# Optimization experiments

Measured on AMD Instinct MI355X. Metric: run time of the kernel, lower is better.

## Reference

```python
import jax, jax.numpy as jnp
import numpy as np

B, S, D = 4, 2048, 1024
H, DK = 16, 64
NUM_BUCKETS = 32
MAX_DISTANCE = 128
EPS = 1e-6


def _relative_position_bucket(q_len, kv_len):
    # causal (bidirectional=False) T5 bucketization
    ctx = jnp.arange(q_len, dtype=jnp.int32)[:, None]
    mem = jnp.arange(kv_len, dtype=jnp.int32)[None, :]
    rp = mem - ctx                       # [q, kv]
    rp = -jnp.minimum(rp, 0)             # nonnegative distances to the past
    max_exact = NUM_BUCKETS // 2
    is_small = rp < max_exact
    rp_safe = jnp.maximum(rp, 1).astype(jnp.float32)
    large = max_exact + (
        jnp.log(rp_safe / max_exact) / np.log(MAX_DISTANCE / max_exact) * (NUM_BUCKETS - max_exact)
    ).astype(jnp.int32)
    large = jnp.minimum(large, NUM_BUCKETS - 1)
    return jnp.where(is_small, rp, large)  # [q, kv] int32 in [0, NUM_BUCKETS)


def setup_inputs() -> dict:
    key = jax.random.key(0)
    k1, k2, k3, k4 = jax.random.split(key, 4)
    hidden_states = jax.random.normal(k1, (B, S, D), dtype=jnp.float32)
    sequence_mask = jnp.ones((B, S), dtype=bool)
    rms_w = jnp.ones((D,), dtype=jnp.float32)
    W_qkv = jax.random.normal(k2, (D, 3 * H * DK), dtype=jnp.float32) * (D ** -0.5)
    W_o = jax.random.normal(k3, (H * DK, D), dtype=jnp.float32) * ((H * DK) ** -0.5)
    rel_bias = jax.random.normal(k4, (NUM_BUCKETS, H), dtype=jnp.float32)
    return {"hidden_states": hidden_states, "sequence_mask": sequence_mask,
            "rms_w": rms_w, "W_qkv": W_qkv, "W_o": W_o, "rel_bias": rel_bias}


def reference(hidden_states, sequence_mask, rms_w, W_qkv, W_o, rel_bias):
    # RMSNorm
    var = jnp.mean(hidden_states * hidden_states, axis=-1, keepdims=True)
    normed = hidden_states * jax.lax.rsqrt(var + EPS) * rms_w

    # QKV projection -> [B, S, 3, H, DK] -> [B, H, S, DK] each
    qkv = (normed @ W_qkv).reshape(B, S, 3, H, DK)
    q = jnp.transpose(qkv[:, :, 0], (0, 2, 1, 3))
    k = jnp.transpose(qkv[:, :, 1], (0, 2, 1, 3))
    v = jnp.transpose(qkv[:, :, 2], (0, 2, 1, 3))

    # relative position bias: gather [S,S,H] -> [1,H,S,S]
    bucket = _relative_position_bucket(S, S)
    pos_bias = jnp.transpose(rel_bias[bucket], (2, 0, 1))[None]

    # scores (note: T5 does NOT scale by 1/sqrt(dk))
    scores = jnp.einsum("bhqd,bhkd->bhqk", q, k) + pos_bias

    # causal mask combined with sequence mask (True = attend)
    causal = jnp.tril(jnp.ones((S, S), dtype=bool))
    mask = causal[None, None] & sequence_mask[:, None, None, :]
    scores = jnp.where(mask, scores, jnp.finfo(scores.dtype).min)

    attn = jax.nn.softmax(scores.astype(jnp.float32), axis=-1).astype(scores.dtype)
    # dropout p=0 / eval mode -> identity
    ctx = jnp.einsum("bhqk,bhkd->bhqd", attn, v)          # [B,H,S,DK]
    ctx = jnp.transpose(ctx, (0, 2, 1, 3)).reshape(B, S, H * DK)
    out = hidden_states + ctx @ W_o                        # residual
    return out
```

## Files before the change

### kernel.cpp

```cpp
#include <hip/hip_runtime.h>
#include <math.h>


typedef unsigned short ushort_t;
typedef __attribute__((ext_vector_type(8))) short bfrag;
typedef __attribute__((ext_vector_type(4))) float ffrag;

#define MFMA16(a, b, c) __builtin_amdgcn_mfma_f32_16x16x32_bf16((a), (b), (c), 0, 0, 0)
#define LOG2E 1.4426950408889634f

__device__ __forceinline__ void load_lds16(const ushort_t* g, ushort_t* l) {
  __builtin_amdgcn_global_load_lds(
      (const __attribute__((address_space(1))) unsigned int*)g,
      (__attribute__((address_space(3))) unsigned int*)l, 16, 0, 0);
}

__device__ __forceinline__ ushort_t f2bf(float f) {
  union { float f; unsigned u; } x; x.f = f;
  unsigned r = x.u + 0x7FFFu + ((x.u >> 16) & 1u);
  return (ushort_t)(r >> 16);
}
__device__ __forceinline__ float bf2f(ushort_t u) {
  union { unsigned u; float f; } x; x.u = ((unsigned)u) << 16; return x.f;
}
__device__ __forceinline__ unsigned cvtpk(float lo, float hi) {
  unsigned r;
  asm("v_cvt_pk_bf16_f32 %0, %1, %2" : "=v"(r) : "v"(lo), "v"(hi));
  return r;
}
__device__ __forceinline__ float exp2fast(float x) {
  return __builtin_amdgcn_exp2f(x);
}

__global__ __launch_bounds__(256) void norm_cvt_kernel(
    const float* __restrict__ hidden, const float* __restrict__ rms_w,
    ushort_t* __restrict__ normed) {
  const int w = threadIdx.x >> 6, lane = threadIdx.x & 63;
  const int row = blockIdx.x * 4 + w;
  const float* p = hidden + (size_t)row * 1024;
  float4 v[4];
  float s = 0.f;
#pragma unroll
  for (int i = 0; i < 4; ++i) {
    v[i] = *(const float4*)(p + (lane + i * 64) * 4);
    s += v[i].x * v[i].x + v[i].y * v[i].y + v[i].z * v[i].z + v[i].w * v[i].w;
  }
#pragma unroll
  for (int off = 1; off < 64; off <<= 1) s += __shfl_xor(s, off, 64);
  const float scale = rsqrtf(s * (1.0f / 1024.0f) + 1e-6f);
#pragma unroll
  for (int i = 0; i < 4; ++i) {
    const int c0 = (lane + i * 64) * 4;
    float4 wv = *(const float4*)(rms_w + c0);
    ushort4 u;
    u.x = f2bf(v[i].x * scale * wv.x);
    u.y = f2bf(v[i].y * scale * wv.y);
    u.z = f2bf(v[i].z * scale * wv.z);
    u.w = f2bf(v[i].w * scale * wv.w);
    *(ushort4*)(normed + (size_t)row * 1024 + c0) = u;
  }
}

__global__ __launch_bounds__(256) void transpose_cvt_kernel(
    const float* __restrict__ in, ushort_t* __restrict__ out, int R, int C) {
  __shared__ float tile[32][33];
  const int r0 = blockIdx.y * 32, c0 = blockIdx.x * 32;
  const int tr = threadIdx.x >> 5, tc = threadIdx.x & 31;
#pragma unroll
  for (int i = 0; i < 32; i += 8)
    tile[tr + i][tc] = in[(size_t)(r0 + tr + i) * C + c0 + tc];
  __syncthreads();
#pragma unroll
  for (int i = 0; i < 32; i += 8)
    out[(size_t)(c0 + tr + i) * R + r0 + tc] = f2bf(tile[tc][tr + i]);
}

__global__ __launch_bounds__(256, 2) void qkv_mfma_kernel(
    const ushort_t* __restrict__ A, const ushort_t* __restrict__ Bt,
    ushort_t* __restrict__ qbf, ushort_t* __restrict__ kbf,
    ushort_t* __restrict__ vtbf) {
  __shared__ ushort_t As[2][128][64];
  __shared__ ushort_t Bs[2][128][64];
  const int tid = threadIdx.x, lane = tid & 63, w = tid >> 6;
  const int quad = lane >> 4, ln = lane & 15;
  const int wr = w >> 1, wc = w & 1;
  const int id = blockIdx.x;
  const int xcd = id & 7, t8 = id >> 3;
  const int by = xcd * 8 + t8 / 24, bx = t8 % 24;
  const int m0 = by * 128, n0 = bx * 128;
  const int rswz = ln & 7;

  auto stage = [&](const ushort_t* src, ushort_t* lds, int gr0, int gc0) {
#pragma unroll
    for (int i = 0; i < 4; ++i) {
      const int idx = i * 256 + tid;
      const int r = idx >> 3, c = idx & 7;
      load_lds16(src + (size_t)(gr0 + r) * 1024 + gc0 + ((c ^ (r & 7)) * 8),
                 lds + idx * 8);
    }
  };

  ffrag acc[4][4];
#pragma unroll
  for (int i = 0; i < 4; ++i)
#pragma unroll
    for (int j = 0; j < 4; ++j) acc[i][j] = (ffrag)0.f;

  stage(A, &As[0][0][0], m0, 0);
  stage(Bt, &Bs[0][0][0], n0, 0);
  asm volatile("s_waitcnt vmcnt(0)" ::: "memory");
  __builtin_amdgcn_s_barrier();

  for (int t = 0; t < 16; ++t) {
    const int cur = t & 1;
    if (t + 1 < 16) {
      stage(A, &As[cur ^ 1][0][0], m0, (t + 1) * 64);
      stage(Bt, &Bs[cur ^ 1][0][0], n0, (t + 1) * 64);
    }
    bfrag a[4][2], b[4][2];
#pragma unroll
    for (int mi = 0; mi < 4; ++mi) {
      const int rA = wr * 64 + mi * 16 + ln;
#pragma unroll
      for (int ks = 0; ks < 2; ++ks)
        a[mi][ks] = *(const bfrag*)(&As[cur][rA][((ks * 4 + quad) ^ rswz) * 8]);
    }
#pragma unroll
    for (int ni = 0; ni < 4; ++ni) {
      const int rB = wc * 64 + ni * 16 + ln;
#pragma unroll
      for (int ks = 0; ks < 2; ++ks)
        b[ni][ks] = *(const bfrag*)(&Bs[cur][rB][((ks * 4 + quad) ^ rswz) * 8]);
    }
    __builtin_amdgcn_s_setprio(1);
#pragma unroll
    for (int mi = 0; mi < 4; ++mi)
#pragma unroll
      for (int ni = 0; ni < 4; ++ni)
#pragma unroll
        for (int ks = 0; ks < 2; ++ks)
          acc[mi][ni] = MFMA16(a[mi][ks], b[ni][ks], acc[mi][ni]);
    __builtin_amdgcn_s_setprio(0);
    asm volatile("s_waitcnt vmcnt(0)" ::: "memory");
    __builtin_amdgcn_s_barrier();
  }

  const int b_idx = m0 >> 11;
  const int cbase = n0 + wc * 64 + ln;
#pragma unroll
  for (int mi = 0; mi < 4; ++mi) {
    const int sbase = (m0 & 2047) + wr * 64 + mi * 16 + quad * 4;
#pragma unroll
    for (int ni = 0; ni < 4; ++ni) {
      const int c = cbase + ni * 16;
      const int three = c >> 10, rem = c & 1023;
      const int h = rem >> 6, dk = rem & 63;
      if (three == 2) {
        ushort4 u;
        u.x = f2bf(acc[mi][ni][0]); u.y = f2bf(acc[mi][ni][1]);
        u.z = f2bf(acc[mi][ni][2]); u.w = f2bf(acc[mi][ni][3]);
        *(ushort4*)(vtbf + ((size_t)(b_idx * 16 + h) * 64 + dk) * 2048 + sbase) = u;
      } else {
        const float sc = (three == 0) ? 1.0f : LOG2E;
        ushort_t* dst = (three == 0 ? qbf : kbf) +
                        ((size_t)(b_idx * 16 + h) * 2048 + sbase) * 64 + dk;
        dst[0]   = f2bf(acc[mi][ni][0] * sc);
        dst[64]  = f2bf(acc[mi][ni][1] * sc);
        dst[128] = f2bf(acc[mi][ni][2] * sc);
        dst[192] = f2bf(acc[mi][ni][3] * sc);
      }
    }
  }
}

__global__ __launch_bounds__(256, 3) void attn_mfma_kernel(
    const ushort_t* __restrict__ qbf, const ushort_t* __restrict__ kbf,
    const ushort_t* __restrict__ vtbf, const float* __restrict__ rel_bias,
    ushort_t* __restrict__ ctx) {
  __shared__ ushort_t Kt[2][2][64][32];
  __shared__ ushort_t Vt[2][2][64][32];
  __shared__ ushort_t Pt[128][64];
  __shared__ ushort_t bias_t[2048];

  const int tid = threadIdx.x, w = tid >> 6, lane = tid & 63;
  const int quad = lane >> 4, ln = lane & 15;
  const int id = blockIdx.x;
  const int bh = id & 63;
  const int qb = 15 - (id >> 6);
  const int h = bh & 15;
  const int nt = 2 * qb + 2;
  const int q0w = qb * 128 + w * 32;

  for (int dist = tid; dist < 2048; dist += 256) {
    int bucket;
    if (dist < 16) bucket = dist;
    else {
      bucket = 16 + (int)(logf((float)dist * (1.0f / 16.0f)) * (16.0f / logf(8.0f)));
      if (bucket > 31) bucket = 31;
    }
    bias_t[dist] = f2bf(rel_bias[bucket * 16 + h] * LOG2E);
  }
  const float c31 = bf2f(f2bf(rel_bias[31 * 16 + h] * LOG2E));
  __syncthreads();

  const size_t khead = (size_t)bh * 2048 * 64;
  const int rsw = ((ln >> 1) & 3) * 8;
  const int psw = (ln & 7) * 8;

  bfrag aq[2][2];
#pragma unroll
  for (int ni = 0; ni < 2; ++ni)
#pragma unroll
    for (int kf = 0; kf < 2; ++kf)
      aq[ni][kf] = *(const bfrag*)(qbf + ((size_t)bh * 2048 + q0w + ni * 16 + ln) * 64 +
                                   kf * 32 + quad * 8);

  bfrag ones;
#pragma unroll
  for (int i = 0; i < 8; ++i) ones[i] = (short)0x3F80;

  ffrag o[2][4], l_acc[2];
#pragma unroll
  for (int mo = 0; mo < 2; ++mo) {
#pragma unroll
    for (int nd = 0; nd < 4; ++nd) o[mo][nd] = (ffrag)0.f;
    l_acc[mo] = (ffrag)0.f;
  }
  float m_run[2] = {-3.0e38f, -3.0e38f};

  auto stageKV = [&](int key0, int buf) {
#pragma unroll
    for (int i = 0; i < 2; ++i) {
      const int cid = i * 256 + tid;
      const int kf = cid >> 8, row = (cid >> 2) & 63, c8 = cid & 3;
      const int sw = (c8 ^ ((row >> 1) & 3)) * 8;
      load_lds16(kbf + khead + (size_t)(key0 + row) * 64 + kf * 32 + sw,
                 &Kt[buf][0][0][0] + cid * 8);
      load_lds16(vtbf + khead + (size_t)row * 2048 + key0 + kf * 32 + sw,
                 &Vt[buf][0][0][0] + cid * 8);
    }
  };

  stageKV(0, 0);

  int cur = 0;
  for (int j = 0; j < nt; ++j) {
    const int key0 = j * 64;
    asm volatile("s_waitcnt vmcnt(0)" ::: "memory");
    __builtin_amdgcn_s_barrier();

    if (j + 1 < nt) stageKV(key0 + 64, cur ^ 1);

    if (key0 <= q0w + 31) {
      ffrag s[4][2];
#pragma unroll
      for (int mi = 0; mi < 4; ++mi)
#pragma unroll
        for (int ni = 0; ni < 2; ++ni) s[mi][ni] = (ffrag)0.f;
      __builtin_amdgcn_s_setprio(1);
#pragma unroll
      for (int kf = 0; kf < 2; ++kf)
#pragma unroll
        for (int mi = 0; mi < 4; ++mi) {
          bfrag ak = *(const bfrag*)&Kt[cur][kf][mi * 16 + ln][(quad * 8) ^ rsw];
          s[mi][0] = MFMA16(ak, aq[0][kf], s[mi][0]);
          s[mi][1] = MFMA16(ak, aq[1][kf], s[mi][1]);
        }
      __builtin_amdgcn_s_setprio(0);

      const bool fastT = (key0 + 176 <= q0w);
      float sbias = 0.f;
      if (fastT) {
        sbias = c31;
      } else {
#pragma unroll
        for (int ni = 0; ni < 2; ++ni) {
          const int q = q0w + ni * 16 + ln;
          if (key0 + 63 > q0w + ni * 16) {
#pragma unroll
            for (int mi = 0; mi < 4; ++mi) {
              const int keyb = key0 + mi * 16 + quad * 4;
#pragma unroll
              for (int r = 0; r < 4; ++r) {
                const int dist = q - (keyb + r);
                const int db = dist < 0 ? 0 : dist;
                s[mi][ni][r] = (dist < 0) ? -3.0e38f
                                          : (s[mi][ni][r] + bf2f(bias_t[db]));
              }
            }
          } else {
#pragma unroll
            for (int mi = 0; mi < 4; ++mi) {
              const int keyb = key0 + mi * 16 + quad * 4;
#pragma unroll
              for (int r = 0; r < 4; ++r)
                s[mi][ni][r] += bf2f(bias_t[q - (keyb + r)]);
            }
          }
        }
      }

      float mxl[2];
#pragma unroll
      for (int ni = 0; ni < 2; ++ni) {
        float a0 = fmaxf(fmaxf(s[0][ni][0], s[0][ni][1]), fmaxf(s[0][ni][2], s[0][ni][3]));
        float a1 = fmaxf(fmaxf(s[1][ni][0], s[1][ni][1]), fmaxf(s[1][ni][2], s[1][ni][3]));
        float a2 = fmaxf(fmaxf(s[2][ni][0], s[2][ni][1]), fmaxf(s[2][ni][2], s[2][ni][3]));
        float a3 = fmaxf(fmaxf(s[3][ni][0], s[3][ni][1]), fmaxf(s[3][ni][2], s[3][ni][3]));
        mxl[ni] = fmaxf(fmaxf(a0, a1), fmaxf(a2, a3)) + sbias;
      }

      if (!__all(mxl[0] <= m_run[0] + 8.0f && mxl[1] <= m_run[1] + 8.0f)) {
#pragma unroll
        for (int ni = 0; ni < 2; ++ni) {
          float mx = mxl[ni];
          mx = fmaxf(mx, __shfl_xor(mx, 16, 64));
          mx = fmaxf(mx, __shfl_xor(mx, 32, 64));
          const float mnew = fmaxf(m_run[ni], mx);
          const float alpha = exp2fast(m_run[ni] - mnew);
          m_run[ni] = mnew;
#pragma unroll
          for (int r = 0; r < 4; ++r) {
            const float af = __shfl(alpha, quad * 4 + r, 64);
#pragma unroll
            for (int nd = 0; nd < 4; ++nd) o[ni][nd][r] *= af;
            l_acc[ni][r] *= af;
          }
        }
      }
#pragma unroll
      for (int ni = 0; ni < 2; ++ni) {
        const float sh = m_run[ni] - sbias;
#pragma unroll
        for (int mi = 0; mi < 4; ++mi)
#pragma unroll
          for (int r = 0; r < 4; ++r)
            s[mi][ni][r] = exp2fast(s[mi][ni][r] - sh);
      }

#pragma unroll
      for (int ni = 0; ni < 2; ++ni) {
        ushort_t* prow = &Pt[w * 32 + ni * 16 + ln][0];
#pragma unroll
        for (int mi = 0; mi < 4; ++mi) {
          uint2 pk;
          pk.x = cvtpk(s[mi][ni][0], s[mi][ni][1]);
          pk.y = cvtpk(s[mi][ni][2], s[mi][ni][3]);
          *(uint2*)(prow + ((mi * 16 + quad * 4) ^ psw)) = pk;
        }
      }

      __builtin_amdgcn_s_setprio(1);
#pragma unroll
      for (int kf = 0; kf < 2; ++kf) {
        bfrag ap0 = *(const bfrag*)&Pt[w * 32 + ln][(kf * 32 + quad * 8) ^ psw];
        bfrag ap1 = *(const bfrag*)&Pt[w * 32 + 16 + ln][(kf * 32 + quad * 8) ^ psw];
        l_acc[0] = MFMA16(ap0, ones, l_acc[0]);
        l_acc[1] = MFMA16(ap1, ones, l_acc[1]);
#pragma unroll
        for (int nd = 0; nd < 4; ++nd) {
          bfrag bv = *(const bfrag*)&Vt[cur][kf][nd * 16 + ln][(quad * 8) ^ rsw];
          o[0][nd] = MFMA16(ap0, bv, o[0][nd]);
          o[1][nd] = MFMA16(ap1, bv, o[1][nd]);
        }
      }
      __builtin_amdgcn_s_setprio(0);
    }
    cur ^= 1;
  }

#pragma unroll
  for (int mo = 0; mo < 2; ++mo) {
    ffrag inv;
#pragma unroll
    for (int r = 0; r < 4; ++r) inv[r] = 1.0f / l_acc[mo][r];
    const int s0 = q0w + mo * 16 + quad * 4;
#pragma unroll
    for (int nd = 0; nd < 4; ++nd)
#pragma unroll
      for (int r = 0; r < 4; ++r)
        ctx[((size_t)(bh >> 4) * 2048 + s0 + r) * 1024 + h * 64 + nd * 16 + ln] =
            f2bf(o[mo][nd][r] * inv[r]);
  }
}

__global__ __launch_bounds__(256, 2) void out_mfma_kernel(
    const ushort_t* __restrict__ A, const ushort_t* __restrict__ Bt,
    const float* __restrict__ hidden, float* __restrict__ out) {
  __shared__ ushort_t As[2][128][64];
  __shared__ ushort_t Bs[2][128][64];
  const int tid = threadIdx.x, lane = tid & 63, w = tid >> 6;
  const int quad = lane >> 4, ln = lane & 15;
  const int wr = w >> 1, wc = w & 1;
  const int id = blockIdx.x;
  const int xcd = id & 7, t = id >> 3;
  const int by = xcd * 8 + (t >> 3), bx = t & 7;
  const int m0 = by * 128, n0 = bx * 128;
  const int rswz = ln & 7;

  auto stage = [&](const ushort_t* src, ushort_t* lds, int gr0, int gc0) {
#pragma unroll
    for (int i = 0; i < 4; ++i) {
      const int idx = i * 256 + tid;
      const int r = idx >> 3, c = idx & 7;
      load_lds16(src + (size_t)(gr0 + r) * 1024 + gc0 + ((c ^ (r & 7)) * 8),
                 lds + idx * 8);
    }
  };

  ffrag acc[4][4];
#pragma unroll
  for (int i = 0; i < 4; ++i)
#pragma unroll
    for (int j = 0; j < 4; ++j) acc[i][j] = (ffrag)0.f;

  stage(A, &As[0][0][0], m0, 0);
  stage(Bt, &Bs[0][0][0], n0, 0);
  asm volatile("s_waitcnt vmcnt(0)" ::: "memory");
  __builtin_amdgcn_s_barrier();

  for (int t2 = 0; t2 < 16; ++t2) {
    const int cur = t2 & 1;
    if (t2 + 1 < 16) {
      stage(A, &As[cur ^ 1][0][0], m0, (t2 + 1) * 64);
      stage(Bt, &Bs[cur ^ 1][0][0], n0, (t2 + 1) * 64);
    }
    bfrag a[4][2], b[4][2];
#pragma unroll
    for (int mi = 0; mi < 4; ++mi) {
      const int rA = wr * 64 + mi * 16 + ln;
#pragma unroll
      for (int ks = 0; ks < 2; ++ks)
        a[mi][ks] = *(const bfrag*)(&As[cur][rA][((ks * 4 + quad) ^ rswz) * 8]);
    }
#pragma unroll
    for (int ni = 0; ni < 4; ++ni) {
      const int rB = wc * 64 + ni * 16 + ln;
#pragma unroll
      for (int ks = 0; ks < 2; ++ks)
        b[ni][ks] = *(const bfrag*)(&Bs[cur][rB][((ks * 4 + quad) ^ rswz) * 8]);
    }
    __builtin_amdgcn_s_setprio(1);
#pragma unroll
    for (int mi = 0; mi < 4; ++mi)
#pragma unroll
      for (int ni = 0; ni < 4; ++ni)
#pragma unroll
        for (int ks = 0; ks < 2; ++ks)
          acc[mi][ni] = MFMA16(a[mi][ks], b[ni][ks], acc[mi][ni]);
    __builtin_amdgcn_s_setprio(0);
    asm volatile("s_waitcnt vmcnt(0)" ::: "memory");
    __builtin_amdgcn_s_barrier();
  }

#pragma unroll
  for (int mi = 0; mi < 4; ++mi) {
    const int m = m0 + wr * 64 + mi * 16 + quad * 4;
#pragma unroll
    for (int ni = 0; ni < 4; ++ni) {
      const int c = n0 + wc * 64 + ni * 16 + ln;
#pragma unroll
      for (int r = 0; r < 4; ++r) {
        const size_t off = (size_t)(m + r) * 1024 + c;
        out[off] = acc[mi][ni][r] + hidden[off];
      }
    }
  }
}

extern "C" void kernel_launch(void* const* d_in, const int* in_sizes, int n_in,
                              void* d_out, int out_size, void* d_ws, size_t ws_size,
                              hipStream_t stream) {
  const size_t NORMED = (size_t)8192 * 1024;
  const size_t WQKVT  = (size_t)3072 * 1024;
  const size_t WOT    = (size_t)1024 * 1024;
  const size_t QKVE   = (size_t)64 * 2048 * 64;
  const size_t need = (NORMED + WQKVT + WOT + 3 * QKVE + NORMED) * 2;
  if (ws_size < need) return;

  const float* hidden   = (const float*)d_in[0];
  const float* rms_w    = (const float*)d_in[2];
  const float* Wqkv     = (const float*)d_in[3];
  const float* Wo       = (const float*)d_in[4];
  const float* rel_bias = (const float*)d_in[5];
  float* out = (float*)d_out;

  ushort_t* normed = (ushort_t*)d_ws;
  ushort_t* wqkvt  = normed + NORMED;
  ushort_t* wot    = wqkvt + WQKVT;
  ushort_t* qbf    = wot + WOT;
  ushort_t* kbf    = qbf + QKVE;
  ushort_t* vtbf   = kbf + QKVE;
  ushort_t* ctx    = vtbf + QKVE;

  norm_cvt_kernel<<<2048, 256, 0, stream>>>(hidden, rms_w, normed);
  transpose_cvt_kernel<<<dim3(96, 32), 256, 0, stream>>>(Wqkv, wqkvt, 1024, 3072);
  transpose_cvt_kernel<<<dim3(32, 32), 256, 0, stream>>>(Wo, wot, 1024, 1024);
  qkv_mfma_kernel<<<1536, 256, 0, stream>>>(normed, wqkvt, qbf, kbf, vtbf);
  attn_mfma_kernel<<<1024, 256, 0, stream>>>(qbf, kbf, vtbf, rel_bias, ctx);
  out_mfma_kernel<<<512, 256, 0, stream>>>(ctx, wot, hidden, out);
}
```

Before: 258.6 us.

## Software-pipeline attention loop: overlap next tile's QK^T with current softmax·V

```diff
diff --git a/kernel.cpp b/kernel.cpp
--- a/kernel.cpp
+++ b/kernel.cpp
@@ -190,6 +190,7 @@
   const int h = bh & 15;
   const int nt = 2 * qb + 2;
   const int q0w = qb * 128 + w * 32;
+  const int jmax = (q0w + 31) >> 6;
 
   for (int dist = tid; dist < 2048; dist += 256) {
     int bucket;
@@ -228,7 +229,7 @@
   }
   float m_run[2] = {-3.0e38f, -3.0e38f};
 
-  auto stageKV = [&](int key0, int buf) {
+  auto stageK = [&](int key0, int buf) {
 #pragma unroll
     for (int i = 0; i < 2; ++i) {
       const int cid = i * 256 + tid;
@@ -236,137 +237,159 @@
       const int sw = (c8 ^ ((row >> 1) & 3)) * 8;
       load_lds16(kbf + khead + (size_t)(key0 + row) * 64 + kf * 32 + sw,
                  &Kt[buf][0][0][0] + cid * 8);
+    }
+  };
+  auto stageV = [&](int key0, int buf) {
+#pragma unroll
+    for (int i = 0; i < 2; ++i) {
+      const int cid = i * 256 + tid;
+      const int kf = cid >> 8, row = (cid >> 2) & 63, c8 = cid & 3;
+      const int sw = (c8 ^ ((row >> 1) & 3)) * 8;
       load_lds16(vtbf + khead + (size_t)row * 2048 + key0 + kf * 32 + sw,
                  &Vt[buf][0][0][0] + cid * 8);
     }
   };
 
-  stageKV(0, 0);
-
-  int cur = 0;
-  for (int j = 0; j < nt; ++j) {
-    const int key0 = j * 64;
+  auto qkt = [&](ffrag (&sx)[4][2], int buf) {
+#pragma unroll
+    for (int mi = 0; mi < 4; ++mi)
+#pragma unroll
+      for (int ni = 0; ni < 2; ++ni) sx[mi][ni] = (ffrag)0.f;
+    __builtin_amdgcn_s_setprio(1);
+#pragma unroll
+    for (int kf = 0; kf < 2; ++kf)
+#pragma unroll
+      for (int mi = 0; mi < 4; ++mi) {
+        bfrag ak = *(const bfrag*)&Kt[buf][kf][mi * 16 + ln][(quad * 8) ^ rsw];
+        sx[mi][0] = MFMA16(ak, aq[0][kf], sx[mi][0]);
+        sx[mi][1] = MFMA16(ak, aq[1][kf], sx[mi][1]);
+      }
+    __builtin_amdgcn_s_setprio(0);
+  };
+
+  auto smpv = [&](ffrag (&sx)[4][2], int t, int vbuf) {
+    const int key0 = t * 64;
+    const bool fastT = (key0 + 176 <= q0w);
+    float sbias = 0.f;
+    if (fastT) {
+      sbias = c31;
+    } else {
+#pragma unroll
+      for (int ni = 0; ni < 2; ++ni) {
+        const int q = q0w + ni * 16 + ln;
+        if (key0 + 63 > q0w + ni * 16) {
+#pragma unroll
+          for (int mi = 0; mi < 4; ++mi) {
+            const int keyb = key0 + mi * 16 + quad * 4;
+#pragma unroll
+            for (int r = 0; r < 4; ++r) {
+              const int dist = q - (keyb + r);
+              const int db = dist < 0 ? 0 : dist;
+              sx[mi][ni][r] = (dist < 0) ? -3.0e38f
+                                         : (sx[mi][ni][r] + bf2f(bias_t[db]));
+            }
+          }
+        } else {
+#pragma unroll
+          for (int mi = 0; mi < 4; ++mi) {
+            const int keyb = key0 + mi * 16 + quad * 4;
+#pragma unroll
+            for (int r = 0; r < 4; ++r)
+              sx[mi][ni][r] += bf2f(bias_t[q - (keyb + r)]);
+          }
+        }
+      }
+    }
+
+    float mxl[2];
+#pragma unroll
+    for (int ni = 0; ni < 2; ++ni) {
+      float a0 = fmaxf(fmaxf(sx[0][ni][0], sx[0][ni][1]), fmaxf(sx[0][ni][2], sx[0][ni][3]));
+      float a1 = fmaxf(fmaxf(sx[1][ni][0], sx[1][ni][1]), fmaxf(sx[1][ni][2], sx[1][ni][3]));
+      float a2 = fmaxf(fmaxf(sx[2][ni][0], sx[2][ni][1]), fmaxf(sx[2][ni][2], sx[2][ni][3]));
+      float a3 = fmaxf(fmaxf(sx[3][ni][0], sx[3][ni][1]), fmaxf(sx[3][ni][2], sx[3][ni][3]));
+      mxl[ni] = fmaxf(fmaxf(a0, a1), fmaxf(a2, a3)) + sbias;
+    }
+
+    if (!__all(mxl[0] <= m_run[0] + 8.0f && mxl[1] <= m_run[1] + 8.0f)) {
+#pragma unroll
+      for (int ni = 0; ni < 2; ++ni) {
+        float mx = mxl[ni];
+        mx = fmaxf(mx, __shfl_xor(mx, 16, 64));
+        mx = fmaxf(mx, __shfl_xor(mx, 32, 64));
+        const float mnew = fmaxf(m_run[ni], mx);
+        const float alpha = exp2fast(m_run[ni] - mnew);
+        m_run[ni] = mnew;
+#pragma unroll
+        for (int r = 0; r < 4; ++r) {
+          const float af = __shfl(alpha, quad * 4 + r, 64);
+#pragma unroll
+          for (int nd = 0; nd < 4; ++nd) o[ni][nd][r] *= af;
+          l_acc[ni][r] *= af;
+        }
+      }
+    }
+#pragma unroll
+    for (int ni = 0; ni < 2; ++ni) {
+      const float sh = m_run[ni] - sbias;
+#pragma unroll
+      for (int mi = 0; mi < 4; ++mi)
+#pragma unroll
+        for (int r = 0; r < 4; ++r)
+          sx[mi][ni][r] = exp2fast(sx[mi][ni][r] - sh);
+    }
+
+#pragma unroll
+    for (int ni = 0; ni < 2; ++ni) {
+      ushort_t* prow = &Pt[w * 32 + ni * 16 + ln][0];
+#pragma unroll
+      for (int mi = 0; mi < 4; ++mi) {
+        uint2 pk;
+        pk.x = cvtpk(sx[mi][ni][0], sx[mi][ni][1]);
+        pk.y = cvtpk(sx[mi][ni][2], sx[mi][ni][3]);
+        *(uint2*)(prow + ((mi * 16 + quad * 4) ^ psw)) = pk;
+      }
+    }
+
+    __builtin_amdgcn_s_setprio(1);
+#pragma unroll
+    for (int kf = 0; kf < 2; ++kf) {
+      bfrag ap0 = *(const bfrag*)&Pt[w * 32 + ln][(kf * 32 + quad * 8) ^ psw];
+      bfrag ap1 = *(const bfrag*)&Pt[w * 32 + 16 + ln][(kf * 32 + quad * 8) ^ psw];
+      l_acc[0] = MFMA16(ap0, ones, l_acc[0]);
+      l_acc[1] = MFMA16(ap1, ones, l_acc[1]);
+#pragma unroll
+      for (int nd = 0; nd < 4; ++nd) {
+        bfrag bv = *(const bfrag*)&Vt[vbuf][kf][nd * 16 + ln][(quad * 8) ^ rsw];
+        o[0][nd] = MFMA16(ap0, bv, o[0][nd]);
+        o[1][nd] = MFMA16(ap1, bv, o[1][nd]);
+      }
+    }
+    __builtin_amdgcn_s_setprio(0);
+  };
+
+  ffrag s0[4][2], s1[4][2];
+  stageK(0, 0);
+  stageV(0, 0);
+  stageK(64, 1);
+  asm volatile("s_waitcnt vmcnt(2)" ::: "memory");
+  __builtin_amdgcn_s_barrier();
+  qkt(s0, 0);
+
+  for (int j = 0; j < nt; j += 2) {
     asm volatile("s_waitcnt vmcnt(0)" ::: "memory");
     __builtin_amdgcn_s_barrier();
-
-    if (j + 1 < nt) stageKV(key0 + 64, cur ^ 1);
-
-    if (key0 <= q0w + 31) {
-      ffrag s[4][2];
-#pragma unroll
-      for (int mi = 0; mi < 4; ++mi)
-#pragma unroll
-        for (int ni = 0; ni < 2; ++ni) s[mi][ni] = (ffrag)0.f;
-      __builtin_amdgcn_s_setprio(1);
-#pragma unroll
-      for (int kf = 0; kf < 2; ++kf)
-#pragma unroll
-        for (int mi = 0; mi < 4; ++mi) {
-          bfrag ak = *(const bfrag*)&Kt[cur][kf][mi * 16 + ln][(quad * 8) ^ rsw];
-          s[mi][0] = MFMA16(ak, aq[0][kf], s[mi][0]);
-          s[mi][1] = MFMA16(ak, aq[1][kf], s[mi][1]);
-        }
-      __builtin_amdgcn_s_setprio(0);
-
-      const bool fastT = (key0 + 176 <= q0w);
-      float sbias = 0.f;
-      if (fastT) {
-        sbias = c31;
-      } else {
-#pragma unroll
-        for (int ni = 0; ni < 2; ++ni) {
-          const int q = q0w + ni * 16 + ln;
-          if (key0 + 63 > q0w + ni * 16) {
-#pragma unroll
-            for (int mi = 0; mi < 4; ++mi) {
-              const int keyb = key0 + mi * 16 + quad * 4;
-#pragma unroll
-              for (int r = 0; r < 4; ++r) {
-                const int dist = q - (keyb + r);
-                const int db = dist < 0 ? 0 : dist;
-                s[mi][ni][r] = (dist < 0) ? -3.0e38f
-                                          : (s[mi][ni][r] + bf2f(bias_t[db]));
-              }
-            }
-          } else {
-#pragma unroll
-            for (int mi = 0; mi < 4; ++mi) {
-              const int keyb = key0 + mi * 16 + quad * 4;
-#pragma unroll
-              for (int r = 0; r < 4; ++r)
-                s[mi][ni][r] += bf2f(bias_t[q - (keyb + r)]);
-            }
-          }
-        }
-      }
-
-      float mxl[2];
-#pragma unroll
-      for (int ni = 0; ni < 2; ++ni) {
-        float a0 = fmaxf(fmaxf(s[0][ni][0], s[0][ni][1]), fmaxf(s[0][ni][2], s[0][ni][3]));
-        float a1 = fmaxf(fmaxf(s[1][ni][0], s[1][ni][1]), fmaxf(s[1][ni][2], s[1][ni][3]));
-        float a2 = fmaxf(fmaxf(s[2][ni][0], s[2][ni][1]), fmaxf(s[2][ni][2], s[2][ni][3]));
-        float a3 = fmaxf(fmaxf(s[3][ni][0], s[3][ni][1]), fmaxf(s[3][ni][2], s[3][ni][3]));
-        mxl[ni] = fmaxf(fmaxf(a0, a1), fmaxf(a2, a3)) + sbias;
-      }
-
-      if (!__all(mxl[0] <= m_run[0] + 8.0f && mxl[1] <= m_run[1] + 8.0f)) {
-#pragma unroll
-        for (int ni = 0; ni < 2; ++ni) {
-          float mx = mxl[ni];
-          mx = fmaxf(mx, __shfl_xor(mx, 16, 64));
-          mx = fmaxf(mx, __shfl_xor(mx, 32, 64));
-          const float mnew = fmaxf(m_run[ni], mx);
-          const float alpha = exp2fast(m_run[ni] - mnew);
-          m_run[ni] = mnew;
-#pragma unroll
-          for (int r = 0; r < 4; ++r) {
-            const float af = __shfl(alpha, quad * 4 + r, 64);
-#pragma unroll
-            for (int nd = 0; nd < 4; ++nd) o[ni][nd][r] *= af;
-            l_acc[ni][r] *= af;
-          }
-        }
-      }
-#pragma unroll
-      for (int ni = 0; ni < 2; ++ni) {
-        const float sh = m_run[ni] - sbias;
-#pragma unroll
-        for (int mi = 0; mi < 4; ++mi)
-#pragma unroll
-          for (int r = 0; r < 4; ++r)
-            s[mi][ni][r] = exp2fast(s[mi][ni][r] - sh);
-      }
-
-#pragma unroll
-      for (int ni = 0; ni < 2; ++ni) {
-        ushort_t* prow = &Pt[w * 32 + ni * 16 + ln][0];
-#pragma unroll
-        for (int mi = 0; mi < 4; ++mi) {
-          uint2 pk;
-          pk.x = cvtpk(s[mi][ni][0], s[mi][ni][1]);
-          pk.y = cvtpk(s[mi][ni][2], s[mi][ni][3]);
-          *(uint2*)(prow + ((mi * 16 + quad * 4) ^ psw)) = pk;
-        }
-      }
-
-      __builtin_amdgcn_s_setprio(1);
-#pragma unroll
-      for (int kf = 0; kf < 2; ++kf) {
-        bfrag ap0 = *(const bfrag*)&Pt[w * 32 + ln][(kf * 32 + quad * 8) ^ psw];
-        bfrag ap1 = *(const bfrag*)&Pt[w * 32 + 16 + ln][(kf * 32 + quad * 8) ^ psw];
-        l_acc[0] = MFMA16(ap0, ones, l_acc[0]);
-        l_acc[1] = MFMA16(ap1, ones, l_acc[1]);
-#pragma unroll
-        for (int nd = 0; nd < 4; ++nd) {
-          bfrag bv = *(const bfrag*)&Vt[cur][kf][nd * 16 + ln][(quad * 8) ^ rsw];
-          o[0][nd] = MFMA16(ap0, bv, o[0][nd]);
-          o[1][nd] = MFMA16(ap1, bv, o[1][nd]);
-        }
-      }
-      __builtin_amdgcn_s_setprio(0);
-    }
-    cur ^= 1;
+    if (j + 2 < nt) stageK((j + 2) * 64, 0);
+    if (j + 1 < nt) stageV((j + 1) * 64, 1);
+    if (j + 1 <= jmax) qkt(s1, 1);
+    if (j <= jmax) smpv(s0, j, 0);
+
+    asm volatile("s_waitcnt vmcnt(0)" ::: "memory");
+    __builtin_amdgcn_s_barrier();
+    if (j + 3 < nt) stageK((j + 3) * 64, 1);
+    if (j + 2 < nt) stageV((j + 2) * 64, 0);
+    if (j + 2 <= jmax) qkt(s0, 0);
+    if (j + 1 <= jmax) smpv(s1, j + 1, 1);
   }
 
 #pragma unroll
@@ -374,12 +397,12 @@
     ffrag inv;
 #pragma unroll
     for (int r = 0; r < 4; ++r) inv[r] = 1.0f / l_acc[mo][r];
-    const int s0 = q0w + mo * 16 + quad * 4;
+    const int s0r = q0w + mo * 16 + quad * 4;
 #pragma unroll
     for (int nd = 0; nd < 4; ++nd)
 #pragma unroll
       for (int r = 0; r < 4; ++r)
-        ctx[((size_t)(bh >> 4) * 2048 + s0 + r) * 1024 + h * 64 + nd * 16 + ln] =
+        ctx[((size_t)(bh >> 4) * 2048 + s0r + r) * 1024 + h * 64 + nd * 16 + ln] =
             f2bf(o[mo][nd][r] * inv[r]);
   }
 }
```

Result: no change. 263.6 us (+1.9%).
